# Performance work log

Hardware: AMD Instinct MI355X
Metric: run time of the kernel (lower is better)

The kernel has to match this reference:

```python
import jax, jax.numpy as jnp
import numpy as np

L, B, C, H, K = 2048, 2, 1024, 16, 9
FF = 4 * C  # conv FFN hidden channels


def _layer_norm(x, w, b, eps=1e-5):
    mu = jnp.mean(x, axis=-1, keepdims=True)
    var = jnp.mean((x - mu) ** 2, axis=-1, keepdims=True)
    return (x - mu) * jax.lax.rsqrt(var + eps) * w + b


def setup_inputs() -> dict:
    key = jax.random.key(0)
    ks = jax.random.split(key, 8)
    s = 0.02  # init scale for weights
    return {
        "x": jax.random.normal(ks[0], (L, B, C), dtype=jnp.float32),
        "mask": jnp.zeros((B, L), dtype=bool),
        "in_proj_w": jax.random.normal(ks[1], (3 * C, C), dtype=jnp.float32) * s,
        "in_proj_b": jnp.zeros((3 * C,), dtype=jnp.float32),
        "out_proj_w": jax.random.normal(ks[2], (C, C), dtype=jnp.float32) * s,
        "out_proj_b": jnp.zeros((C,), dtype=jnp.float32),
        "conv1_w": jax.random.normal(ks[3], (FF, C, K), dtype=jnp.float32) * s,
        "conv1_b": jnp.zeros((FF,), dtype=jnp.float32),
        "conv2_w": jax.random.normal(ks[4], (C, FF, 1), dtype=jnp.float32) * s,
        "conv2_b": jnp.zeros((C,), dtype=jnp.float32),
        "norm1_w": jnp.ones((C,), dtype=jnp.float32),
        "norm1_b": jnp.zeros((C,), dtype=jnp.float32),
        "norm2_w": jnp.ones((C,), dtype=jnp.float32),
        "norm2_b": jnp.zeros((C,), dtype=jnp.float32),
    }


def reference(x, mask, in_proj_w, in_proj_b, out_proj_w, out_proj_b,
              conv1_w, conv1_b, conv2_w, conv2_b,
              norm1_w, norm1_b, norm2_w, norm2_b):
    hd = C // H
    # --- self-attention ---
    qkv = x @ in_proj_w.T + in_proj_b            # (L, B, 3C)
    q, k, v = jnp.split(qkv, 3, axis=-1)

    def heads(t):  # (L, B, C) -> (B, H, L, hd)
        return t.reshape(L, B, H, hd).transpose(1, 2, 0, 3)

    q, k, v = heads(q), heads(k), heads(v)
    scores = jnp.einsum('bhqd,bhkd->bhqk', q, k) / jnp.sqrt(jnp.float32(hd))
    scores = jnp.where(mask[:, None, None, :], -jnp.inf, scores)
    attn = jax.nn.softmax(scores, axis=-1)
    ao = jnp.einsum('bhqk,bhkd->bhqd', attn, v)  # (B, H, L, hd)
    ao = ao.transpose(2, 0, 1, 3).reshape(L, B, C)
    ao = ao @ out_proj_w.T + out_proj_b
    x1 = _layer_norm(x + ao, norm1_w, norm1_b)
    # --- conv feed-forward ---
    xc = x1.transpose(1, 2, 0)                   # (B, C, L)
    dn = ('NCH', 'OIH', 'NCH')
    h = jax.lax.conv_general_dilated(xc, conv1_w, (1,), [(K // 2, K // 2)],
                                     dimension_numbers=dn)
    h = jax.nn.relu(h + conv1_b[None, :, None])
    h = jax.lax.conv_general_dilated(h, conv2_w, (1,), [(0, 0)],
                                     dimension_numbers=dn)
    h = h + conv2_b[None, :, None]
    return _layer_norm(x1 + h.transpose(2, 0, 1), norm2_w, norm2_b)
```

## Files before the change

kernel.cpp:

```cpp
#include <hip/hip_runtime.h>
#include <cstdint>
#include <cstddef>

#define LSEQ 2048
#define NB   2
#define CCH  1024
#define NHD  16
#define HDD  64
#define FFC  4096
#define KW   9
#define MROWS 4096

typedef __bf16 bf16x8 __attribute__((ext_vector_type(8)));
typedef float  floatx4 __attribute__((ext_vector_type(4)));
typedef unsigned short ushort4v __attribute__((ext_vector_type(4)));

__device__ inline unsigned short f2bf(float f) {
  union { float f; unsigned u; } v; v.f = f;
  unsigned r = v.u + 0x7FFFu + ((v.u >> 16) & 1u);
  return (unsigned short)(r >> 16);
}

__device__ inline void gload_lds16(const unsigned short* g, unsigned short* l) {
  __builtin_amdgcn_global_load_lds(
      (__attribute__((address_space(1))) unsigned int*)(g),
      (__attribute__((address_space(3))) unsigned int*)(l), 16, 0, 0);
}

__global__ void f2bf4_kernel(const float* __restrict__ in, unsigned short* __restrict__ out, int n4) {
  int idx = blockIdx.x * 256 + threadIdx.x;
  if (idx >= n4) return;
  const floatx4 v = ((const floatx4*)in)[idx];
  unsigned long long pk = (unsigned long long)f2bf(v[0]) |
                          ((unsigned long long)f2bf(v[1]) << 16) |
                          ((unsigned long long)f2bf(v[2]) << 32) |
                          ((unsigned long long)f2bf(v[3]) << 48);
  ((unsigned long long*)out)[idx] = pk;
}

__global__ __launch_bounds__(256) void repack_w1_kernel(const float* __restrict__ in,
                                                        unsigned short* __restrict__ out) {
  __shared__ unsigned short t[9216];
  const int f = blockIdx.x, tid = threadIdx.x;
  const float* src = in + (size_t)f * 9216;
#pragma unroll
  for (int rnd = 0; rnd < 9; ++rnd) {
    const int p = (rnd * 256 + tid) * 4;
    const floatx4 v = *(const floatx4*)(src + p);
#pragma unroll
    for (int e = 0; e < 4; ++e) {
      const int idx = p + e;
      const int c = idx / 9, k = idx - c * 9;
      t[k * 1024 + c] = f2bf(v[e]);
    }
  }
  __syncthreads();
  unsigned short* dst = out + (size_t)f * 9216;
#pragma unroll
  for (int rnd = 0; rnd < 9; ++rnd) {
    const int j = (rnd * 256 + tid) * 4;
    *(ushort4v*)(dst + j) = *(const ushort4v*)&t[j];
  }
}

__global__ void zero_u16(unsigned short* p, int n) {
  int idx = blockIdx.x * 256 + threadIdx.x;
  if (idx < n) p[idx] = 0;
}

template <int EPI, bool KDEC, int BN>
__global__ __launch_bounds__(256) void gemm_bt(
    const unsigned short* __restrict__ A, const unsigned short* __restrict__ Bm,
    const float* __restrict__ bias, int N, int K,
    float* __restrict__ outF, unsigned short* __restrict__ outB,
    unsigned short* __restrict__ qb, unsigned short* __restrict__ kb,
    unsigned short* __restrict__ vtb) {
  constexpr int JN = BN / 32;
  __shared__ alignas(16) unsigned short lA[128 * 32];
  __shared__ alignas(16) unsigned short lB[BN * 32];
  const int tid = threadIdx.x;
  const int m0 = blockIdx.x * 128;
  const int n0 = blockIdx.y * BN;
  const int wave = tid >> 6, lane = tid & 63;
  const int wm = (wave >> 1) * 64, wn = (wave & 1) * (BN / 2);
  const int l16 = lane & 15, quad = lane >> 4;
  const int fsw = (quad ^ ((l16 >> 1) & 3)) << 3;

  size_t aoff[2], boff[BN / 64];
#pragma unroll
  for (int i = 0; i < 2; ++i) {
    const int flat = i * 256 + tid;
    const int row = flat >> 2, cs = flat & 3;
    const int col = ((cs ^ ((row >> 1) & 3)) << 3);
    aoff[i] = (KDEC ? (size_t)row * 1024 : (size_t)(m0 + row) * K) + col;
  }
#pragma unroll
  for (int i = 0; i < BN / 64; ++i) {
    const int flat = i * 256 + tid;
    const int row = flat >> 2, cs = flat & 3;
    const int col = ((cs ^ ((row >> 1) & 3)) << 3);
    boff[i] = (size_t)(n0 + row) * K + col;
  }

  floatx4 acc[4][JN];
#pragma unroll
  for (int i = 0; i < 4; ++i)
#pragma unroll
    for (int j = 0; j < JN; ++j) acc[i][j] = (floatx4){0.f, 0.f, 0.f, 0.f};

  auto kstep = [&](const unsigned short* Ab, const unsigned short* Bb) {
    __syncthreads();
#pragma unroll
    for (int i = 0; i < 2; ++i)
      gload_lds16(Ab + aoff[i], &lA[(i * 256 + tid) * 8]);
#pragma unroll
    for (int i = 0; i < BN / 64; ++i)
      gload_lds16(Bb + boff[i], &lB[(i * 256 + tid) * 8]);
    __syncthreads();
    bf16x8 af[4], bf[JN];
#pragma unroll
    for (int i = 0; i < 4; ++i)
      af[i] = *(const bf16x8*)&lA[(wm + i * 16 + l16) * 32 + fsw];
#pragma unroll
    for (int j = 0; j < JN; ++j)
      bf[j] = *(const bf16x8*)&lB[(wn + j * 16 + l16) * 32 + fsw];
#pragma unroll
    for (int i = 0; i < 4; ++i)
#pragma unroll
      for (int j = 0; j < JN; ++j)
        acc[i][j] = __builtin_amdgcn_mfma_f32_16x16x32_bf16(af[i], bf[j], acc[i][j], 0, 0, 0);
  };

  if (KDEC) {
    for (int seg = 0; seg < KW; ++seg) {
      const unsigned short* Ab = A + (size_t)(m0 + seg * NB) * 1024;
      const unsigned short* Bb = Bm + seg * 1024;
      for (int kk = 0; kk < 1024; kk += 32) kstep(Ab + kk, Bb + kk);
    }
  } else {
    for (int k0 = 0; k0 < K; k0 += 32) kstep(A + k0, Bm + k0);
  }

#pragma unroll
  for (int i = 0; i < 4; ++i) {
#pragma unroll
    for (int j = 0; j < JN; ++j) {
      const int colg = n0 + wn + j * 16 + l16;
      const int rbase = m0 + wm + i * 16 + quad * 4;
      float vv[4];
#pragma unroll
      for (int r = 0; r < 4; ++r) vv[r] = acc[i][j][r] + bias[colg];
      if (EPI == 1) {
#pragma unroll
        for (int r = 0; r < 4; ++r) outF[(size_t)(rbase + r) * N + colg] = vv[r];
      } else if (EPI == 2) {
#pragma unroll
        for (int r = 0; r < 4; ++r)
          outB[(size_t)(rbase + r) * N + colg] = f2bf(fmaxf(vv[r], 0.f));
      } else {
        if (colg < 1024) {
          const int h = colg >> 6, d = colg & 63;
#pragma unroll
          for (int r = 0; r < 4; ++r) {
            const int row = rbase + r, l = row >> 1, b = row & 1;
            qb[(((size_t)(b * NHD + h)) * LSEQ + l) * HDD + d] = f2bf(vv[r] * 0.125f);
          }
        } else if (colg < 2048) {
          const int c = colg - 1024, h = c >> 6, d = c & 63;
#pragma unroll
          for (int r = 0; r < 4; ++r) {
            const int row = rbase + r, l = row >> 1, b = row & 1;
            kb[(((size_t)(b * NHD + h)) * LSEQ + l) * HDD + d] = f2bf(vv[r]);
          }
        } else {
          const int c = colg - 2048, h = c >> 6, d = c & 63;
#pragma unroll
          for (int rp = 0; rp < 2; ++rp) {
            const int row = rbase + rp, l = row >> 1, b = row & 1;
            const unsigned lo = f2bf(vv[rp]), hi = f2bf(vv[rp + 2]);
            *(unsigned*)&vtb[(((size_t)(b * NHD + h)) * HDD + d) * LSEQ + l] =
                lo | (hi << 16);
          }
        }
      }
    }
  }
}

__global__ __launch_bounds__(256) void attn_kernel(
    const unsigned short* __restrict__ qg, const unsigned short* __restrict__ kg,
    const unsigned short* __restrict__ vtg, unsigned short* __restrict__ ao) {
  __shared__ alignas(16) unsigned short lK[64 * 64];
  __shared__ alignas(16) unsigned short lV[64 * 64];
  __shared__ alignas(16) unsigned short lP[4][16 * 64];
  const int tid = threadIdx.x;
  const int wave = tid >> 6, lane = tid & 63;
  const int l16 = lane & 15, quad = lane >> 4;
  const int sw0 = ((quad ^ (l16 & 7)) << 3);
  const int sw1 = (((quad | 4) ^ (l16 & 7)) << 3);
  const int qt = blockIdx.x, h = blockIdx.y, b = blockIdx.z;
  const unsigned short* Q = qg + ((size_t)(b * NHD + h) * LSEQ) * HDD;
  const unsigned short* Kp = kg + ((size_t)(b * NHD + h) * LSEQ) * HDD;
  const unsigned short* Vt = vtg + ((size_t)(b * NHD + h) * HDD) * LSEQ;
  const int q0 = qt * 64 + wave * 16;

  const bf16x8 qa0 = *(const bf16x8*)&Q[(size_t)(q0 + l16) * HDD + quad * 8];
  const bf16x8 qa1 = *(const bf16x8*)&Q[(size_t)(q0 + l16) * HDD + 32 + quad * 8];

  float mr[4], lr[4];
  floatx4 o[4];
#pragma unroll
  for (int r = 0; r < 4; ++r) { mr[r] = -1e30f; lr[r] = 0.f; }
#pragma unroll
  for (int nb = 0; nb < 4; ++nb) o[nb] = (floatx4){0.f, 0.f, 0.f, 0.f};

  for (int kt = 0; kt < LSEQ; kt += 64) {
    __syncthreads();
#pragma unroll
    for (int i = 0; i < 2; ++i) {
      const int flat = i * 256 + tid;
      const int row = flat >> 3, cs = flat & 7;
      const int col = ((cs ^ (row & 7)) << 3);
      gload_lds16(&Kp[(size_t)(kt + row) * HDD + col], &lK[flat * 8]);
      gload_lds16(&Vt[(size_t)row * LSEQ + kt + col], &lV[flat * 8]);
    }
    __syncthreads();
    floatx4 s[4];
#pragma unroll
    for (int nb = 0; nb < 4; ++nb) {
      const bf16x8 kf0 = *(const bf16x8*)&lK[(nb * 16 + l16) * 64 + sw0];
      const bf16x8 kf1 = *(const bf16x8*)&lK[(nb * 16 + l16) * 64 + sw1];
      floatx4 t = (floatx4){0.f, 0.f, 0.f, 0.f};
      t = __builtin_amdgcn_mfma_f32_16x16x32_bf16(qa0, kf0, t, 0, 0, 0);
      t = __builtin_amdgcn_mfma_f32_16x16x32_bf16(qa1, kf1, t, 0, 0, 0);
      s[nb] = t;
    }
    float mnew[4], alpha[4];
#pragma unroll
    for (int r = 0; r < 4; ++r) {
      float mx = fmaxf(fmaxf(s[0][r], s[1][r]), fmaxf(s[2][r], s[3][r]));
      mx = fmaxf(mx, __shfl_xor(mx, 1));
      mx = fmaxf(mx, __shfl_xor(mx, 2));
      mx = fmaxf(mx, __shfl_xor(mx, 4));
      mx = fmaxf(mx, __shfl_xor(mx, 8));
      mnew[r] = fmaxf(mr[r], mx);
      alpha[r] = __expf(mr[r] - mnew[r]);
      mr[r] = mnew[r];
    }
#pragma unroll
    for (int nb = 0; nb < 4; ++nb)
#pragma unroll
      for (int r = 0; r < 4; ++r) s[nb][r] = __expf(s[nb][r] - mnew[r]);
#pragma unroll
    for (int r = 0; r < 4; ++r) {
      float sm = s[0][r] + s[1][r] + s[2][r] + s[3][r];
      sm += __shfl_xor(sm, 1);
      sm += __shfl_xor(sm, 2);
      sm += __shfl_xor(sm, 4);
      sm += __shfl_xor(sm, 8);
      lr[r] = lr[r] * alpha[r] + sm;
    }
#pragma unroll
    for (int nb = 0; nb < 4; ++nb)
#pragma unroll
      for (int r = 0; r < 4; ++r) {
        const int row = quad * 4 + r;
        const int q = nb * 2 + (l16 >> 3);
        lP[wave][row * 64 + ((q ^ (row & 7)) << 3) + (l16 & 7)] = f2bf(s[nb][r]);
        o[nb][r] *= alpha[r];
      }
    asm volatile("s_waitcnt lgkmcnt(0)" ::: "memory");
    const bf16x8 pa0 = *(const bf16x8*)&lP[wave][l16 * 64 + sw0];
    const bf16x8 pa1 = *(const bf16x8*)&lP[wave][l16 * 64 + sw1];
#pragma unroll
    for (int nb = 0; nb < 4; ++nb) {
      const bf16x8 vf0 = *(const bf16x8*)&lV[(nb * 16 + l16) * 64 + sw0];
      const bf16x8 vf1 = *(const bf16x8*)&lV[(nb * 16 + l16) * 64 + sw1];
      o[nb] = __builtin_amdgcn_mfma_f32_16x16x32_bf16(pa0, vf0, o[nb], 0, 0, 0);
      o[nb] = __builtin_amdgcn_mfma_f32_16x16x32_bf16(pa1, vf1, o[nb], 0, 0, 0);
    }
  }
#pragma unroll
  for (int nb = 0; nb < 4; ++nb)
#pragma unroll
    for (int r = 0; r < 4; ++r) {
      const float v = o[nb][r] / lr[r];
      const int lg = q0 + quad * 4 + r;
      ao[((size_t)lg * NB + b) * CCH + h * HDD + nb * 16 + l16] = f2bf(v);
    }
}

__global__ __launch_bounds__(256) void ln_kernel(
    const float* __restrict__ a, const float* __restrict__ c,
    const float* __restrict__ w, const float* __restrict__ bias,
    float* __restrict__ outF, unsigned short* __restrict__ outB) {
  const int row = blockIdx.x;
  const int tid = threadIdx.x;
  const floatx4 va = *(const floatx4*)(a + (size_t)row * 1024 + tid * 4);
  const floatx4 vc = *(const floatx4*)(c + (size_t)row * 1024 + tid * 4);
  float v0 = va[0] + vc[0], v1 = va[1] + vc[1], v2 = va[2] + vc[2], v3 = va[3] + vc[3];
  float s = v0 + v1 + v2 + v3;
  float ss = v0 * v0 + v1 * v1 + v2 * v2 + v3 * v3;
#pragma unroll
  for (int off = 1; off < 64; off <<= 1) {
    s += __shfl_xor(s, off);
    ss += __shfl_xor(ss, off);
  }
  __shared__ float red[8];
  const int wave = tid >> 6, lane = tid & 63;
  if (lane == 0) { red[wave] = s; red[4 + wave] = ss; }
  __syncthreads();
  s = red[0] + red[1] + red[2] + red[3];
  ss = red[4] + red[5] + red[6] + red[7];
  const float mu = s * (1.f / 1024.f);
  const float var = ss * (1.f / 1024.f) - mu * mu;
  const float rs = rsqrtf(var + 1e-5f);
  const floatx4 wv = *(const floatx4*)(w + tid * 4);
  const floatx4 bv = *(const floatx4*)(bias + tid * 4);
  const float o0 = (v0 - mu) * rs * wv[0] + bv[0];
  const float o1 = (v1 - mu) * rs * wv[1] + bv[1];
  const float o2 = (v2 - mu) * rs * wv[2] + bv[2];
  const float o3 = (v3 - mu) * rs * wv[3] + bv[3];
  *(floatx4*)(outF + (size_t)row * 1024 + tid * 4) = (floatx4){o0, o1, o2, o3};
  if (outB) {
    unsigned long long pk = (unsigned long long)f2bf(o0) |
                            ((unsigned long long)f2bf(o1) << 16) |
                            ((unsigned long long)f2bf(o2) << 32) |
                            ((unsigned long long)f2bf(o3) << 48);
    *(unsigned long long*)(outB + (size_t)row * 1024 + tid * 4) = pk;
  }
}

extern "C" void kernel_launch(void* const* d_in, const int* in_sizes, int n_in,
                              void* d_out, int out_size, void* d_ws, size_t ws_size,
                              hipStream_t stream) {
  const float* x = (const float*)d_in[0];
  const float* wqkv = (const float*)d_in[2];
  const float* bqkv = (const float*)d_in[3];
  const float* wout = (const float*)d_in[4];
  const float* bout = (const float*)d_in[5];
  const float* w1 = (const float*)d_in[6];
  const float* b1 = (const float*)d_in[7];
  const float* w2 = (const float*)d_in[8];
  const float* b2 = (const float*)d_in[9];
  const float* n1w = (const float*)d_in[10];
  const float* n1b = (const float*)d_in[11];
  const float* n2w = (const float*)d_in[12];
  const float* n2b = (const float*)d_in[13];
  float* out = (float*)d_out;

  char* ws = (char*)d_ws;
  size_t off = 0;
  auto alloc = [&](size_t bytes) -> char* {
    char* p = ws + off;
    off += (bytes + 255) & ~(size_t)255;
    return p;
  };
  unsigned short* xb    = (unsigned short*)alloc((size_t)MROWS * 1024 * 2);
  unsigned short* wqkvb = (unsigned short*)alloc((size_t)3072 * 1024 * 2);
  unsigned short* woutb = (unsigned short*)alloc((size_t)1024 * 1024 * 2);
  unsigned short* w1p   = (unsigned short*)alloc((size_t)FFC * 9216 * 2);
  unsigned short* w2b   = (unsigned short*)alloc((size_t)1024 * FFC * 2);
  unsigned short* qbuf  = (unsigned short*)alloc((size_t)NB * NHD * LSEQ * HDD * 2);
  unsigned short* kbuf  = (unsigned short*)alloc((size_t)NB * NHD * LSEQ * HDD * 2);
  unsigned short* vtbuf = (unsigned short*)alloc((size_t)NB * NHD * LSEQ * HDD * 2);
  unsigned short* ao    = (unsigned short*)alloc((size_t)MROWS * 1024 * 2);
  float*          yz    = (float*)alloc((size_t)MROWS * 1024 * 4);
  float*          x1f   = (float*)alloc((size_t)MROWS * 1024 * 4);
  unsigned short* x1p   = (unsigned short*)alloc((size_t)(LSEQ + 8) * NB * 1024 * 2);
  unsigned short* hbuf  = (unsigned short*)alloc((size_t)MROWS * FFC * 2);
  if (off > ws_size) return;

  int n;
  n = MROWS * 1024 / 4; f2bf4_kernel<<<(n + 255) / 256, 256, 0, stream>>>(x, xb, n);
  n = 3072 * 1024 / 4;  f2bf4_kernel<<<(n + 255) / 256, 256, 0, stream>>>(wqkv, wqkvb, n);
  n = 1024 * 1024 / 4;  f2bf4_kernel<<<(n + 255) / 256, 256, 0, stream>>>(wout, woutb, n);
  n = 1024 * FFC / 4;   f2bf4_kernel<<<(n + 255) / 256, 256, 0, stream>>>(w2, w2b, n);
  repack_w1_kernel<<<FFC, 256, 0, stream>>>(w1, w1p);
  zero_u16<<<32, 256, 0, stream>>>(x1p, 8 * 1024);
  zero_u16<<<32, 256, 0, stream>>>(x1p + (size_t)(LSEQ + 4) * NB * 1024, 8 * 1024);

  gemm_bt<0, false, 128><<<dim3(32, 24), 256, 0, stream>>>(
      xb, wqkvb, bqkv, 3072, 1024, nullptr, nullptr, qbuf, kbuf, vtbuf);
  attn_kernel<<<dim3(LSEQ / 64, NHD, NB), 256, 0, stream>>>(qbuf, kbuf, vtbuf, ao);
  gemm_bt<1, false, 64><<<dim3(32, 16), 256, 0, stream>>>(
      ao, woutb, bout, 1024, 1024, yz, nullptr, nullptr, nullptr, nullptr);
  ln_kernel<<<MROWS, 256, 0, stream>>>(x, yz, n1w, n1b, x1f, x1p + 8 * 1024);
  gemm_bt<2, true, 128><<<dim3(32, 32), 256, 0, stream>>>(
      x1p, w1p, b1, FFC, 9216, nullptr, hbuf, nullptr, nullptr, nullptr);
  gemm_bt<1, false, 64><<<dim3(32, 16), 256, 0, stream>>>(
      hbuf, w2b, b2, 1024, FFC, yz, nullptr, nullptr, nullptr, nullptr);
  ln_kernel<<<MROWS, 256, 0, stream>>>(x1f, yz, n2w, n2b, out, nullptr);
}
```

Before: 973.9 us.

## Double GEMM K-step to 64 and remap blocks for XCD-local B-tile reuse

The GEMM K tile grows from 32 to 64 bf16 elements per stage, which halves the number of barrier pairs and global-to-LDS rounds per output tile. An 8-way XOR swizzle is added for the wider LDS rows. The grid is flattened and remapped so that blocks landing on the same XCD (flat id mod 8) share a small set of N-column tiles, which is meant to improve L2 reuse of weight tiles. In exchange, LDS use doubles and the kernel is still single-buffered.

```diff
diff --git a/kernel.cpp b/kernel.cpp
--- a/kernel.cpp
+++ b/kernel.cpp
@@ -71,34 +71,40 @@
 template <int EPI, bool KDEC, int BN>
 __global__ __launch_bounds__(256) void gemm_bt(
     const unsigned short* __restrict__ A, const unsigned short* __restrict__ Bm,
-    const float* __restrict__ bias, int N, int K,
+    const float* __restrict__ bias, int N, int K, int NYP,
     float* __restrict__ outF, unsigned short* __restrict__ outB,
     unsigned short* __restrict__ qb, unsigned short* __restrict__ kb,
     unsigned short* __restrict__ vtb) {
   constexpr int JN = BN / 32;
-  __shared__ alignas(16) unsigned short lA[128 * 32];
-  __shared__ alignas(16) unsigned short lB[BN * 32];
+  constexpr int BR = BN / 32;
+  __shared__ alignas(16) unsigned short lA[128 * 64];
+  __shared__ alignas(16) unsigned short lB[BN * 64];
   const int tid = threadIdx.x;
-  const int m0 = blockIdx.x * 128;
-  const int n0 = blockIdx.y * BN;
+  const int flat = blockIdx.x;
+  const int xcd = flat & 7;
+  const int idx = flat >> 3;
+  const int m0 = (idx & 31) * 128;
+  const int n0 = (xcd * NYP + (idx >> 5)) * BN;
   const int wave = tid >> 6, lane = tid & 63;
   const int wm = (wave >> 1) * 64, wn = (wave & 1) * (BN / 2);
   const int l16 = lane & 15, quad = lane >> 4;
-  const int fsw = (quad ^ ((l16 >> 1) & 3)) << 3;
-
-  size_t aoff[2], boff[BN / 64];
-#pragma unroll
-  for (int i = 0; i < 2; ++i) {
-    const int flat = i * 256 + tid;
-    const int row = flat >> 2, cs = flat & 3;
-    const int col = ((cs ^ ((row >> 1) & 3)) << 3);
+  const int e3 = l16 & 7;
+  const int fsw0 = ((quad ^ e3) << 3);
+  const int fsw1 = (((quad | 4) ^ e3) << 3);
+
+  size_t aoff[4], boff[BR];
+#pragma unroll
+  for (int i = 0; i < 4; ++i) {
+    const int cf = i * 256 + tid;
+    const int row = cf >> 3, cs = cf & 7;
+    const int col = ((cs ^ (row & 7)) << 3);
     aoff[i] = (KDEC ? (size_t)row * 1024 : (size_t)(m0 + row) * K) + col;
   }
 #pragma unroll
-  for (int i = 0; i < BN / 64; ++i) {
-    const int flat = i * 256 + tid;
-    const int row = flat >> 2, cs = flat & 3;
-    const int col = ((cs ^ ((row >> 1) & 3)) << 3);
+  for (int i = 0; i < BR; ++i) {
+    const int cf = i * 256 + tid;
+    const int row = cf >> 3, cs = cf & 7;
+    const int col = ((cs ^ (row & 7)) << 3);
     boff[i] = (size_t)(n0 + row) * K + col;
   }
 
@@ -111,19 +117,30 @@
   auto kstep = [&](const unsigned short* Ab, const unsigned short* Bb) {
     __syncthreads();
 #pragma unroll
-    for (int i = 0; i < 2; ++i)
+    for (int i = 0; i < 4; ++i)
       gload_lds16(Ab + aoff[i], &lA[(i * 256 + tid) * 8]);
 #pragma unroll
-    for (int i = 0; i < BN / 64; ++i)
+    for (int i = 0; i < BR; ++i)
       gload_lds16(Bb + boff[i], &lB[(i * 256 + tid) * 8]);
     __syncthreads();
     bf16x8 af[4], bf[JN];
 #pragma unroll
     for (int i = 0; i < 4; ++i)
-      af[i] = *(const bf16x8*)&lA[(wm + i * 16 + l16) * 32 + fsw];
+      af[i] = *(const bf16x8*)&lA[(wm + i * 16 + l16) * 64 + fsw0];
 #pragma unroll
     for (int j = 0; j < JN; ++j)
-      bf[j] = *(const bf16x8*)&lB[(wn + j * 16 + l16) * 32 + fsw];
+      bf[j] = *(const bf16x8*)&lB[(wn + j * 16 + l16) * 64 + fsw0];
+#pragma unroll
+    for (int i = 0; i < 4; ++i)
+#pragma unroll
+      for (int j = 0; j < JN; ++j)
+        acc[i][j] = __builtin_amdgcn_mfma_f32_16x16x32_bf16(af[i], bf[j], acc[i][j], 0, 0, 0);
+#pragma unroll
+    for (int i = 0; i < 4; ++i)
+      af[i] = *(const bf16x8*)&lA[(wm + i * 16 + l16) * 64 + fsw1];
+#pragma unroll
+    for (int j = 0; j < JN; ++j)
+      bf[j] = *(const bf16x8*)&lB[(wn + j * 16 + l16) * 64 + fsw1];
 #pragma unroll
     for (int i = 0; i < 4; ++i)
 #pragma unroll
@@ -135,10 +152,10 @@
     for (int seg = 0; seg < KW; ++seg) {
       const unsigned short* Ab = A + (size_t)(m0 + seg * NB) * 1024;
       const unsigned short* Bb = Bm + seg * 1024;
-      for (int kk = 0; kk < 1024; kk += 32) kstep(Ab + kk, Bb + kk);
+      for (int kk = 0; kk < 1024; kk += 64) kstep(Ab + kk, Bb + kk);
     }
   } else {
-    for (int k0 = 0; k0 < K; k0 += 32) kstep(A + k0, Bm + k0);
+    for (int k0 = 0; k0 < K; k0 += 64) kstep(A + k0, Bm + k0);
   }
 
 #pragma unroll
@@ -380,15 +397,15 @@
   zero_u16<<<32, 256, 0, stream>>>(x1p, 8 * 1024);
   zero_u16<<<32, 256, 0, stream>>>(x1p + (size_t)(LSEQ + 4) * NB * 1024, 8 * 1024);
 
-  gemm_bt<0, false, 128><<<dim3(32, 24), 256, 0, stream>>>(
-      xb, wqkvb, bqkv, 3072, 1024, nullptr, nullptr, qbuf, kbuf, vtbuf);
+  gemm_bt<0, false, 128><<<32 * 24, 256, 0, stream>>>(
+      xb, wqkvb, bqkv, 3072, 1024, 3, nullptr, nullptr, qbuf, kbuf, vtbuf);
   attn_kernel<<<dim3(LSEQ / 64, NHD, NB), 256, 0, stream>>>(qbuf, kbuf, vtbuf, ao);
-  gemm_bt<1, false, 64><<<dim3(32, 16), 256, 0, stream>>>(
-      ao, woutb, bout, 1024, 1024, yz, nullptr, nullptr, nullptr, nullptr);
+  gemm_bt<1, false, 64><<<32 * 16, 256, 0, stream>>>(
+      ao, woutb, bout, 1024, 1024, 2, yz, nullptr, nullptr, nullptr, nullptr);
   ln_kernel<<<MROWS, 256, 0, stream>>>(x, yz, n1w, n1b, x1f, x1p + 8 * 1024);
-  gemm_bt<2, true, 128><<<dim3(32, 32), 256, 0, stream>>>(
-      x1p, w1p, b1, FFC, 9216, nullptr, hbuf, nullptr, nullptr, nullptr);
-  gemm_bt<1, false, 64><<<dim3(32, 16), 256, 0, stream>>>(
-      hbuf, w2b, b2, 1024, FFC, yz, nullptr, nullptr, nullptr, nullptr);
+  gemm_bt<2, true, 128><<<32 * 32, 256, 0, stream>>>(
+      x1p, w1p, b1, FFC, 9216, 4, nullptr, hbuf, nullptr, nullptr, nullptr);
+  gemm_bt<1, false, 64><<<32 * 16, 256, 0, stream>>>(
+      hbuf, w2b, b2, 1024, FFC, 2, yz, nullptr, nullptr, nullptr, nullptr);
   ln_kernel<<<MROWS, 256, 0, stream>>>(x1f, yz, n2w, n2b, out, nullptr);
 }
```

Result: slower. 1.004 ms (+3.1%).

## Split-K the FFN down-projection and write V row-major with a separate transpose

Applied to the files above, without the earlier changes.

The conv2 GEMM (K=4096) is split into two K halves over blockIdx.z, which doubles the block count from 512 to 1024. The two partial sums go to separate fp32 buffers and are added, along with the bias, inside the final LayerNorm. The QKV epilogue now writes V row-major into a scratch buffer instead of doing a strided transposed store, and a new LDS-tiled transpose kernel produces the layout attention expects. This trades an extra kernel launch and extra memory traffic for better occupancy and coalesced stores.

```diff
diff --git a/kernel.cpp b/kernel.cpp
--- a/kernel.cpp
+++ b/kernel.cpp
@@ -68,19 +68,49 @@
   if (idx < n) p[idx] = 0;
 }
 
+__global__ __launch_bounds__(256) void transpose_v_kernel(
+    const unsigned short* __restrict__ vin, unsigned short* __restrict__ vout) {
+  __shared__ unsigned short t[64][65];
+  const int tid = threadIdx.x;
+  const int l0 = blockIdx.x * 64, bh = blockIdx.y;
+  const unsigned short* src = vin + ((size_t)bh * LSEQ + l0) * HDD;
+  const int rr = tid >> 4, cc = (tid & 15) * 4;
+#pragma unroll
+  for (int rnd = 0; rnd < 4; ++rnd) {
+    const int row = rnd * 16 + rr;
+    const ushort4v v = *(const ushort4v*)(src + row * HDD + cc);
+#pragma unroll
+    for (int e = 0; e < 4; ++e) t[row][cc + e] = v[e];
+  }
+  __syncthreads();
+  unsigned short* dst = vout + (size_t)bh * HDD * LSEQ + l0;
+#pragma unroll
+  for (int rnd = 0; rnd < 4; ++rnd) {
+    const int drow = rnd * 16 + rr;
+    ushort4v v;
+#pragma unroll
+    for (int e = 0; e < 4; ++e) v[e] = t[cc + e][drow];
+    *(ushort4v*)(dst + (size_t)drow * LSEQ + cc) = v;
+  }
+}
+
 template <int EPI, bool KDEC, int BN>
 __global__ __launch_bounds__(256) void gemm_bt(
     const unsigned short* __restrict__ A, const unsigned short* __restrict__ Bm,
-    const float* __restrict__ bias, int N, int K,
-    float* __restrict__ outF, unsigned short* __restrict__ outB,
+    const float* __restrict__ bias, int N, int Kstride, int Klen,
+    float* __restrict__ outF, float* __restrict__ outF2,
+    unsigned short* __restrict__ outB,
     unsigned short* __restrict__ qb, unsigned short* __restrict__ kb,
-    unsigned short* __restrict__ vtb) {
+    unsigned short* __restrict__ vb) {
   constexpr int JN = BN / 32;
   __shared__ alignas(16) unsigned short lA[128 * 32];
   __shared__ alignas(16) unsigned short lB[BN * 32];
   const int tid = threadIdx.x;
   const int m0 = blockIdx.x * 128;
   const int n0 = blockIdx.y * BN;
+  const int z = blockIdx.z;
+  A += (size_t)z * Klen;
+  Bm += (size_t)z * Klen;
   const int wave = tid >> 6, lane = tid & 63;
   const int wm = (wave >> 1) * 64, wn = (wave & 1) * (BN / 2);
   const int l16 = lane & 15, quad = lane >> 4;
@@ -89,17 +119,17 @@
   size_t aoff[2], boff[BN / 64];
 #pragma unroll
   for (int i = 0; i < 2; ++i) {
-    const int flat = i * 256 + tid;
-    const int row = flat >> 2, cs = flat & 3;
+    const int cf = i * 256 + tid;
+    const int row = cf >> 2, cs = cf & 3;
     const int col = ((cs ^ ((row >> 1) & 3)) << 3);
-    aoff[i] = (KDEC ? (size_t)row * 1024 : (size_t)(m0 + row) * K) + col;
+    aoff[i] = (KDEC ? (size_t)row * 1024 : (size_t)(m0 + row) * Kstride) + col;
   }
 #pragma unroll
   for (int i = 0; i < BN / 64; ++i) {
-    const int flat = i * 256 + tid;
-    const int row = flat >> 2, cs = flat & 3;
+    const int cf = i * 256 + tid;
+    const int row = cf >> 2, cs = cf & 3;
     const int col = ((cs ^ ((row >> 1) & 3)) << 3);
-    boff[i] = (size_t)(n0 + row) * K + col;
+    boff[i] = (size_t)(n0 + row) * Kstride + col;
   }
 
   floatx4 acc[4][JN];
@@ -138,49 +168,36 @@
       for (int kk = 0; kk < 1024; kk += 32) kstep(Ab + kk, Bb + kk);
     }
   } else {
-    for (int k0 = 0; k0 < K; k0 += 32) kstep(A + k0, Bm + k0);
-  }
-
+    for (int k0 = 0; k0 < Klen; k0 += 32) kstep(A + k0, Bm + k0);
+  }
+
+  float* outZ = (z == 0) ? outF : outF2;
 #pragma unroll
   for (int i = 0; i < 4; ++i) {
 #pragma unroll
     for (int j = 0; j < JN; ++j) {
       const int colg = n0 + wn + j * 16 + l16;
       const int rbase = m0 + wm + i * 16 + quad * 4;
+      const float bv = bias ? bias[colg] : 0.f;
       float vv[4];
 #pragma unroll
-      for (int r = 0; r < 4; ++r) vv[r] = acc[i][j][r] + bias[colg];
+      for (int r = 0; r < 4; ++r) vv[r] = acc[i][j][r] + bv;
       if (EPI == 1) {
 #pragma unroll
-        for (int r = 0; r < 4; ++r) outF[(size_t)(rbase + r) * N + colg] = vv[r];
+        for (int r = 0; r < 4; ++r) outZ[(size_t)(rbase + r) * N + colg] = vv[r];
       } else if (EPI == 2) {
 #pragma unroll
         for (int r = 0; r < 4; ++r)
           outB[(size_t)(rbase + r) * N + colg] = f2bf(fmaxf(vv[r], 0.f));
       } else {
-        if (colg < 1024) {
-          const int h = colg >> 6, d = colg & 63;
-#pragma unroll
-          for (int r = 0; r < 4; ++r) {
-            const int row = rbase + r, l = row >> 1, b = row & 1;
-            qb[(((size_t)(b * NHD + h)) * LSEQ + l) * HDD + d] = f2bf(vv[r] * 0.125f);
-          }
-        } else if (colg < 2048) {
-          const int c = colg - 1024, h = c >> 6, d = c & 63;
-#pragma unroll
-          for (int r = 0; r < 4; ++r) {
-            const int row = rbase + r, l = row >> 1, b = row & 1;
-            kb[(((size_t)(b * NHD + h)) * LSEQ + l) * HDD + d] = f2bf(vv[r]);
-          }
-        } else {
-          const int c = colg - 2048, h = c >> 6, d = c & 63;
-#pragma unroll
-          for (int rp = 0; rp < 2; ++rp) {
-            const int row = rbase + rp, l = row >> 1, b = row & 1;
-            const unsigned lo = f2bf(vv[rp]), hi = f2bf(vv[rp + 2]);
-            *(unsigned*)&vtb[(((size_t)(b * NHD + h)) * HDD + d) * LSEQ + l] =
-                lo | (hi << 16);
-          }
+        const int seg = colg >> 10;
+        const int c = colg & 1023, h = c >> 6, d = c & 63;
+        unsigned short* dst = (seg == 0) ? qb : (seg == 1) ? kb : vb;
+        const float scl = (seg == 0) ? 0.125f : 1.f;
+#pragma unroll
+        for (int r = 0; r < 4; ++r) {
+          const int row = rbase + r, l = row >> 1, b = row & 1;
+          dst[(((size_t)(b * NHD + h)) * LSEQ + l) * HDD + d] = f2bf(vv[r] * scl);
         }
       }
     }
@@ -292,6 +309,7 @@
 
 __global__ __launch_bounds__(256) void ln_kernel(
     const float* __restrict__ a, const float* __restrict__ c,
+    const float* __restrict__ c2, const float* __restrict__ cbias,
     const float* __restrict__ w, const float* __restrict__ bias,
     float* __restrict__ outF, unsigned short* __restrict__ outB) {
   const int row = blockIdx.x;
@@ -299,6 +317,14 @@
   const floatx4 va = *(const floatx4*)(a + (size_t)row * 1024 + tid * 4);
   const floatx4 vc = *(const floatx4*)(c + (size_t)row * 1024 + tid * 4);
   float v0 = va[0] + vc[0], v1 = va[1] + vc[1], v2 = va[2] + vc[2], v3 = va[3] + vc[3];
+  if (c2) {
+    const floatx4 v2c = *(const floatx4*)(c2 + (size_t)row * 1024 + tid * 4);
+    v0 += v2c[0]; v1 += v2c[1]; v2 += v2c[2]; v3 += v2c[3];
+  }
+  if (cbias) {
+    const floatx4 vb = *(const floatx4*)(cbias + tid * 4);
+    v0 += vb[0]; v1 += vb[1]; v2 += vb[2]; v3 += vb[3];
+  }
   float s = v0 + v1 + v2 + v3;
   float ss = v0 * v0 + v1 * v1 + v2 * v2 + v3 * v3;
 #pragma unroll
@@ -370,6 +396,8 @@
   unsigned short* x1p   = (unsigned short*)alloc((size_t)(LSEQ + 8) * NB * 1024 * 2);
   unsigned short* hbuf  = (unsigned short*)alloc((size_t)MROWS * FFC * 2);
   if (off > ws_size) return;
+  float*          yzB   = (float*)xb;
+  unsigned short* vbuf  = hbuf;
 
   int n;
   n = MROWS * 1024 / 4; f2bf4_kernel<<<(n + 255) / 256, 256, 0, stream>>>(x, xb, n);
@@ -381,14 +409,15 @@
   zero_u16<<<32, 256, 0, stream>>>(x1p + (size_t)(LSEQ + 4) * NB * 1024, 8 * 1024);
 
   gemm_bt<0, false, 128><<<dim3(32, 24), 256, 0, stream>>>(
-      xb, wqkvb, bqkv, 3072, 1024, nullptr, nullptr, qbuf, kbuf, vtbuf);
+      xb, wqkvb, bqkv, 3072, 1024, 1024, nullptr, nullptr, nullptr, qbuf, kbuf, vbuf);
+  transpose_v_kernel<<<dim3(LSEQ / 64, NB * NHD), 256, 0, stream>>>(vbuf, vtbuf);
   attn_kernel<<<dim3(LSEQ / 64, NHD, NB), 256, 0, stream>>>(qbuf, kbuf, vtbuf, ao);
   gemm_bt<1, false, 64><<<dim3(32, 16), 256, 0, stream>>>(
-      ao, woutb, bout, 1024, 1024, yz, nullptr, nullptr, nullptr, nullptr);
-  ln_kernel<<<MROWS, 256, 0, stream>>>(x, yz, n1w, n1b, x1f, x1p + 8 * 1024);
+      ao, woutb, bout, 1024, 1024, 1024, yz, nullptr, nullptr, nullptr, nullptr, nullptr);
+  ln_kernel<<<MROWS, 256, 0, stream>>>(x, yz, nullptr, nullptr, n1w, n1b, x1f, x1p + 8 * 1024);
   gemm_bt<2, true, 128><<<dim3(32, 32), 256, 0, stream>>>(
-      x1p, w1p, b1, FFC, 9216, nullptr, hbuf, nullptr, nullptr, nullptr);
-  gemm_bt<1, false, 64><<<dim3(32, 16), 256, 0, stream>>>(
-      hbuf, w2b, b2, 1024, FFC, yz, nullptr, nullptr, nullptr, nullptr);
-  ln_kernel<<<MROWS, 256, 0, stream>>>(x1f, yz, n2w, n2b, out, nullptr);
-}
+      x1p, w1p, b1, FFC, 9216, 9216, nullptr, nullptr, hbuf, nullptr, nullptr, nullptr);
+  gemm_bt<1, false, 64><<<dim3(32, 16, 2), 256, 0, stream>>>(
+      hbuf, w2b, nullptr, 1024, FFC, 2048, yz, yzB, nullptr, nullptr, nullptr, nullptr);
+  ln_kernel<<<MROWS, 256, 0, stream>>>(x1f, yz, yzB, b2, n2w, n2b, out, nullptr);
+}
```

After: 968.8 us. No clear change (-0.5%).
